# Performance work log

Measured on AMD Instinct MI355X. Metric: run time of the kernel, lower is better.

The kernel has to match this reference:

```python
import jax, jax.numpy as jnp
import numpy as np

N = 16384      # total nodes
B = 8          # graphs in batch
NPG = N // B   # nodes per graph
E = 262144     # edges
IN, HID, OUT = 128, 256, 128
ICP_ITERS = 10


def setup_inputs():
    key = jax.random.key(0)
    ks = jax.random.split(key, 12)
    x = jax.random.normal(ks[0], (N, IN), jnp.float32)
    # random edges kept within each graph (offsets per graph)
    src = jax.random.randint(ks[1], (E,), 0, NPG, dtype=jnp.int32)
    dst = jax.random.randint(ks[2], (E,), 0, NPG, dtype=jnp.int32)
    goff = (jnp.arange(E, dtype=jnp.int32) % B) * NPG
    edge_index = jnp.stack([src + goff, dst + goff], 0)
    pos = jax.random.normal(ks[3], (N, 3), jnp.float32)
    batch = jnp.repeat(jnp.arange(B, dtype=jnp.int32), NPG)
    def lin(k, fi, fo):
        return jax.random.normal(k, (fi, fo), jnp.float32) * (fi ** -0.5)
    return dict(
        x=x, edge_index=edge_index, pos=pos, batch=batch,
        W1=lin(ks[4], IN, HID),  b1=jnp.zeros((HID,), jnp.float32),
        W2=lin(ks[5], HID, HID), b2=jnp.zeros((HID,), jnp.float32),
        W3=lin(ks[6], HID, OUT), b3=jnp.zeros((OUT,), jnp.float32),
        Wt=lin(ks[7], OUT, 3),   bt=jnp.zeros((3,), jnp.float32),
    )


def gcn_conv(x, W, b, row, col, n):
    # GCNConv: symmetric norm with self loops; messages flow row->col
    xw = x @ W
    loop = jnp.arange(n, dtype=row.dtype)
    r = jnp.concatenate([row, loop])
    c = jnp.concatenate([col, loop])
    deg = jax.ops.segment_sum(jnp.ones_like(c, dtype=xw.dtype), c, num_segments=n)
    dinv = jnp.where(deg > 0, jax.lax.rsqrt(jnp.maximum(deg, 1e-12)), 0.0)
    norm = dinv[r] * dinv[c]
    out = jax.ops.segment_sum(xw[r] * norm[:, None], c, num_segments=n)
    return out + b


def pdist2(a, b):
    # squared pairwise distances [n,m]
    return (jnp.sum(a * a, -1)[:, None] + jnp.sum(b * b, -1)[None, :]
            - 2.0 * (a @ b.T))


def icp_align(src, tgt):
    # fixed-iteration batched ICP (Kabsch/SVD per iteration)
    for _ in range(ICP_ITERS):
        d = pdist2(jax.lax.stop_gradient(src), jax.lax.stop_gradient(tgt))
        idx = jnp.argmin(d, axis=1)
        corr = tgt[idx]
        cs = jnp.mean(src, 0)
        cc = jnp.mean(corr, 0)
        H = (src - cs).T @ (corr - cc)  # [3,3]
        U, S, Vt = jnp.linalg.svd(H, full_matrices=False)
        sign = jnp.sign(jnp.linalg.det(Vt.T @ U.T))
        D = jnp.stack([jnp.ones_like(sign), jnp.ones_like(sign), sign])
        R = (Vt.T * D[None, :]) @ U.T
        t = cc - R @ cs
        src = src @ R.T + t
    return src


def chamfer(a, b):
    d = pdist2(jax.lax.stop_gradient(a), jax.lax.stop_gradient(b))
    ia = jnp.argmin(d, 1)
    ib = jnp.argmin(d, 0)
    d1 = jnp.mean(jnp.sum((a - b[ia]) ** 2, -1))
    d2 = jnp.mean(jnp.sum((b - a[ib]) ** 2, -1))
    return d1 + d2


def reference(x, edge_index, pos, batch, W1, b1, W2, b2, W3, b3, Wt, bt):
    n = x.shape[0]
    row, col = edge_index[0], edge_index[1]
    h = jax.nn.relu(gcn_conv(x, W1, b1, row, col, n))
    h = jax.nn.relu(gcn_conv(h, W2, b2, row, col, n))
    h = gcn_conv(h, W3, b3, row, col, n)
    pos_offset = h @ Wt + bt
    tpos = pos + pos_offset
    nb = int(batch[-1]) + 1          # sorted, equal-size graphs
    npg = n // nb
    src = tpos.reshape(nb, npg, 3)
    tgt = pos.reshape(nb, npg, 3)
    aligned = jax.vmap(icp_align)(src, tgt)
    loss = jnp.mean(jax.vmap(chamfer)(aligned, tgt))
    return h, aligned.reshape(n, 3), loss
```

## Files before the change

### kernel.cpp

```cpp
#include <hip/hip_runtime.h>
#include <math.h>

#define N_NODES 16384
#define B_GRAPHS 8
#define NPG_     2048
#define E_EDGES  262144
#define F_IN  128
#define F_HID 256
#define F_OUT 128
#define ICP_IT 10
#define NN_BPG 32

typedef __attribute__((ext_vector_type(8))) short bf16x8;
typedef __attribute__((ext_vector_type(4))) float f32x4;

__device__ __forceinline__ float b2f(unsigned short u) {
    union { unsigned int u; float f; } v; v.u = ((unsigned int)u) << 16; return v.f;
}
__device__ __forceinline__ unsigned short f2b(float f) {
    union { float f; unsigned int u; } v; v.f = f;
    unsigned int r = v.u + 0x7FFFu + ((v.u >> 16) & 1u);
    return (unsigned short)(r >> 16);
}
__device__ __forceinline__ int swz32(int i) {
    return (i & ~31) | ((i & 31) ^ ((i >> 5) & 31));
}
__device__ __forceinline__ void st_agent(float* p, float v) {
    __hip_atomic_store(p, v, __ATOMIC_RELAXED, __HIP_MEMORY_SCOPE_AGENT);
}
__device__ __forceinline__ float ld_agent(const float* p) {
    return __hip_atomic_load(p, __ATOMIC_RELAXED, __HIP_MEMORY_SCOPE_AGENT);
}
__device__ __forceinline__ int ld_agent_i(const int* p) {
    return __hip_atomic_load(p, __ATOMIC_RELAXED, __HIP_MEMORY_SCOPE_AGENT);
}

__global__ __launch_bounds__(256) void k_prep(
    const float* __restrict__ x, unsigned short* __restrict__ xb,
    const float* __restrict__ W1, const float* __restrict__ W2, const float* __restrict__ W3,
    unsigned short* __restrict__ W1b, unsigned short* __restrict__ W2b, unsigned short* __restrict__ W3b,
    int* __restrict__ counts, int* __restrict__ ctrs)
{
    const int b = blockIdx.x, tid = threadIdx.x;
    if (b < 2048) {
        int i = b * 256 + tid;
        float4 v = ((const float4*)x)[i];
        uint2 o;
        o.x = (unsigned int)f2b(v.x) | ((unsigned int)f2b(v.y) << 16);
        o.y = (unsigned int)f2b(v.z) | ((unsigned int)f2b(v.w) << 16);
        ((uint2*)xb)[i] = o;
    } else if (b < 2176) {
        int idx = (b - 2048) * 256 + tid;
        int k = idx >> 8, n = idx & 255;
        W1b[n * 128 + k] = f2b(W1[idx]);
    } else if (b < 2432) {
        int idx = (b - 2176) * 256 + tid;
        int k = idx >> 8, n = idx & 255;
        W2b[n * 256 + k] = f2b(W2[idx]);
    } else if (b < 2560) {
        int idx = (b - 2432) * 256 + tid;
        int k = idx >> 7, n = idx & 127;
        W3b[n * 256 + k] = f2b(W3[idx]);
    } else if (b < 2576) {
        int i = (b - 2560) * 256 + tid;
        ((int4*)counts)[i] = make_int4(0, 0, 0, 0);
    } else {
        ctrs[tid] = 0;
    }
}

__global__ void k_count(const int* __restrict__ col, int* __restrict__ counts) {
    int e = blockIdx.x * 256 + threadIdx.x;
    if (e < E_EDGES) atomicAdd(&counts[col[e]], 1);
}

__global__ __launch_bounds__(1024) void k_scan(const int* __restrict__ counts,
        int* __restrict__ offs, int* __restrict__ cursor, float* __restrict__ dinv)
{
    __shared__ int wtot[16];
    const int t = threadIdx.x;
    const int base = t * 16;
    int local[16];
    int s = 0;
#pragma unroll
    for (int i = 0; i < 16; i++) { local[i] = counts[base + i]; s += local[i]; }
    const int lane = t & 63, w = t >> 6;
    int inc = s;
    for (int o = 1; o < 64; o <<= 1) {
        int v = __shfl_up(inc, o);
        if (lane >= o) inc += v;
    }
    if (lane == 63) wtot[w] = inc;
    __syncthreads();
    if (t < 16) {
        int v = wtot[t];
        for (int o = 1; o < 16; o <<= 1) {
            int u = __shfl_up(v, o);
            if (t >= o) v += u;
        }
        wtot[t] = v;
    }
    __syncthreads();
    int run = (w > 0 ? wtot[w - 1] : 0) + (inc - s);
#pragma unroll
    for (int i = 0; i < 16; i++) {
        offs[base + i]   = run;
        cursor[base + i] = run;
        dinv[base + i]   = rsqrtf((float)(local[i] + 1));
        run += local[i];
    }
    if (t == 1023) offs[N_NODES] = run;
}

__global__ void k_scatter(const int* __restrict__ row, const int* __restrict__ col,
        int* __restrict__ cursor, const float* __restrict__ dinv,
        int* __restrict__ srcid, float* __restrict__ normv)
{
    int e = blockIdx.x * 256 + threadIdx.x;
    if (e >= E_EDGES) return;
    int r = row[e], c = col[e];
    int p = atomicAdd(&cursor[c], 1);
    srcid[p] = r;
    normv[p] = dinv[r] * dinv[c];
}

template<int W, int OUTF, int FUSET>
__global__ __launch_bounds__(128) void k_agg(const unsigned short* __restrict__ X,
        void* __restrict__ Y,
        const int* __restrict__ offs, const int* __restrict__ srcid,
        const float* __restrict__ normv, const float* __restrict__ dinv,
        const float* __restrict__ bias, int relu,
        const float* __restrict__ Wt, const float* __restrict__ bt,
        const float* __restrict__ pos, float* __restrict__ tposO)
{
    constexpr int NPB = (W == 128) ? 2 : 1;
    constexpr int W2 = W / 2;
    const int local = (NPB == 2) ? (threadIdx.x >> 6) : 0;
    const int n = blockIdx.x * NPB + local;
    const int j = (NPB == 2) ? (threadIdx.x & 63) : threadIdx.x;
    const unsigned int* Xu = (const unsigned int*)X;
    float di = dinv[n];
    float w0 = di * di;
    unsigned int v = Xu[(size_t)n * W2 + j];
    float a0 = b2f((unsigned short)v) * w0;
    float a1 = b2f((unsigned short)(v >> 16)) * w0;
    int p = offs[n];
    const int p1 = offs[n + 1];
    for (; p + 3 < p1; p += 4) {
        int s0i = srcid[p], s1i = srcid[p + 1], s2i = srcid[p + 2], s3i = srcid[p + 3];
        float n0 = normv[p], n1 = normv[p + 1], n2 = normv[p + 2], n3 = normv[p + 3];
        unsigned int v0 = Xu[(size_t)s0i * W2 + j];
        unsigned int v1 = Xu[(size_t)s1i * W2 + j];
        unsigned int v2 = Xu[(size_t)s2i * W2 + j];
        unsigned int v3 = Xu[(size_t)s3i * W2 + j];
        a0 = fmaf(b2f((unsigned short)v0), n0, a0);
        a1 = fmaf(b2f((unsigned short)(v0 >> 16)), n0, a1);
        a0 = fmaf(b2f((unsigned short)v1), n1, a0);
        a1 = fmaf(b2f((unsigned short)(v1 >> 16)), n1, a1);
        a0 = fmaf(b2f((unsigned short)v2), n2, a0);
        a1 = fmaf(b2f((unsigned short)(v2 >> 16)), n2, a1);
        a0 = fmaf(b2f((unsigned short)v3), n3, a0);
        a1 = fmaf(b2f((unsigned short)(v3 >> 16)), n3, a1);
    }
    for (; p < p1; ++p) {
        unsigned int va = Xu[(size_t)srcid[p] * W2 + j]; float na = normv[p];
        a0 = fmaf(b2f((unsigned short)va), na, a0);
        a1 = fmaf(b2f((unsigned short)(va >> 16)), na, a1);
    }
    if (bias) { a0 += bias[2 * j]; a1 += bias[2 * j + 1]; }
    if (relu) { a0 = fmaxf(a0, 0.f); a1 = fmaxf(a1, 0.f); }
    if (OUTF) {
        float* Yf = (float*)Y;
        Yf[(size_t)n * W + 2 * j]     = a0;
        Yf[(size_t)n * W + 2 * j + 1] = a1;
    } else {
        ((unsigned int*)Y)[(size_t)n * W2 + j] =
            (unsigned int)f2b(a0) | ((unsigned int)f2b(a1) << 16);
    }
    if (FUSET) {
        float wt0 = Wt[6 * j + 0], wt1 = Wt[6 * j + 1], wt2 = Wt[6 * j + 2];
        float wt3 = Wt[6 * j + 3], wt4 = Wt[6 * j + 4], wt5 = Wt[6 * j + 5];
        float s0 = a0 * wt0 + a1 * wt3;
        float s1 = a0 * wt1 + a1 * wt4;
        float s2 = a0 * wt2 + a1 * wt5;
        for (int o = 32; o > 0; o >>= 1) {
            s0 += __shfl_down(s0, o);
            s1 += __shfl_down(s1, o);
            s2 += __shfl_down(s2, o);
        }
        if (j == 0) {
            tposO[n * 3 + 0] = pos[n * 3 + 0] + s0 + bt[0];
            tposO[n * 3 + 1] = pos[n * 3 + 1] + s1 + bt[1];
            tposO[n * 3 + 2] = pos[n * 3 + 2] + s2 + bt[2];
        }
    }
}

__global__ __launch_bounds__(256) void k_gemm_bf16(
    const unsigned short* __restrict__ A,
    const unsigned short* __restrict__ Bt,
    const float* __restrict__ bias, unsigned short* __restrict__ C,
    int M, int N, int K, int relu)
{
    __shared__ __align__(16) unsigned short As[128 * 64];
    __shared__ __align__(16) unsigned short Bs[64 * 64];
    const int tid  = threadIdx.x;
    const int lane = tid & 63;
    const int wave = tid >> 6;
    const int bm = blockIdx.y * 128, bn = blockIdx.x * 64;
    const int wm = (wave >> 1) * 64, wn = (wave & 1) * 32;
    f32x4 acc[4][2];
#pragma unroll
    for (int mf = 0; mf < 4; mf++)
#pragma unroll
        for (int nf = 0; nf < 2; nf++) acc[mf][nf] = (f32x4){0.f, 0.f, 0.f, 0.f};

    for (int k0 = 0; k0 < K; k0 += 64) {
#pragma unroll
        for (int i = 0; i < 4; i++) {
            int idx = i * 256 + tid;
            int m = idx >> 3, slot = idx & 7;
            const unsigned short* src = A + (size_t)(bm + m) * K + k0 + ((slot ^ (m & 7)) << 3);
            __builtin_amdgcn_global_load_lds(
                (const __attribute__((address_space(1))) unsigned int*)src,
                (__attribute__((address_space(3))) unsigned int*)(As + (size_t)i * 2048 + wave * 512),
                16, 0, 0);
        }
#pragma unroll
        for (int i = 0; i < 2; i++) {
            int idx = i * 256 + tid;
            int n = idx >> 3, slot = idx & 7;
            const unsigned short* src = Bt + (size_t)(bn + n) * K + k0 + ((slot ^ (n & 7)) << 3);
            __builtin_amdgcn_global_load_lds(
                (const __attribute__((address_space(1))) unsigned int*)src,
                (__attribute__((address_space(3))) unsigned int*)(Bs + (size_t)i * 2048 + wave * 512),
                16, 0, 0);
        }
        __syncthreads();
        bf16x8 af[4][2], bfr[2][2];
        const int qd = lane >> 4;
#pragma unroll
        for (int s = 0; s < 2; s++) {
#pragma unroll
            for (int mf = 0; mf < 4; mf++) {
                int m = wm + mf * 16 + (lane & 15);
                int slot = (s * 4 + qd) ^ (m & 7);
                af[mf][s] = *(const bf16x8*)(As + m * 64 + slot * 8);
            }
#pragma unroll
            for (int nf = 0; nf < 2; nf++) {
                int n = wn + nf * 16 + (lane & 15);
                int slot = (s * 4 + qd) ^ (n & 7);
                bfr[nf][s] = *(const bf16x8*)(Bs + n * 64 + slot * 8);
            }
        }
#pragma unroll
        for (int s = 0; s < 2; s++)
#pragma unroll
            for (int mf = 0; mf < 4; mf++)
#pragma unroll
                for (int nf = 0; nf < 2; nf++)
                    acc[mf][nf] = __builtin_amdgcn_mfma_f32_16x16x32_bf16(
                        af[mf][s], bfr[nf][s], acc[mf][nf], 0, 0, 0);
        __syncthreads();
    }
#pragma unroll
    for (int nf = 0; nf < 2; nf++) {
        int col = bn + wn + nf * 16 + (lane & 15);
        float bv = bias ? bias[col] : 0.f;
#pragma unroll
        for (int mf = 0; mf < 4; mf++) {
#pragma unroll
            for (int r = 0; r < 4; r++) {
                int row = bm + wm + mf * 16 + (lane >> 4) * 4 + r;
                float v = acc[mf][nf][r] + bv;
                if (relu) v = fmaxf(v, 0.f);
                C[(size_t)row * N + col] = f2b(v);
            }
        }
    }
}

__global__ __launch_bounds__(512) void k_icp_all(
    const float* __restrict__ tpos, const float* __restrict__ pos,
    float* __restrict__ partials,
    float* __restrict__ chpart,
    int* __restrict__ ctrs,
    float* __restrict__ out_aligned, float* __restrict__ out_loss)
{
    const int g = blockIdx.x >> 5, blk = blockIdx.x & 31;
    const int tid = threadIdx.x;
    const int wave = tid >> 6, lane = tid & 63;
    __shared__ float4 tq[NPG_];
    __shared__ __align__(16) unsigned char scratch[NPG_ * 16];
    float* sm_d = (float*)scratch;
    unsigned short* sm_i = (unsigned short*)(scratch + 64 * 65 * 4);
    float4* al = (float4*)scratch;
    __shared__ float mom[15][33];
    __shared__ float ssx[64], ssy[64], ssz[64];
    __shared__ float wred[16][2];
    __shared__ float Tsh[12];
    __shared__ double sdl[15];
    __shared__ int lastFlag;

    for (int i = tid; i < NPG_; i += 512) {
        const float* p = &pos[(size_t)(g * NPG_ + i) * 3];
        float qx = p[0], qy = p[1], qz = p[2];
        tq[swz32(i)] = make_float4(qx, qy, qz, fmaf(qx, qx, fmaf(qy, qy, qz * qz)));
    }
    if (tid < 12) Tsh[tid] = (tid == 0 || tid == 4 || tid == 8) ? 1.f : 0.f;
    float Px[8], Py[8], Pz[8];
#pragma unroll
    for (int u = 0; u < 8; u++) {
        int n = g * NPG_ + blk * 64 + wave * 8 + u;
        Px[u] = tpos[n * 3 + 0]; Py[u] = tpos[n * 3 + 1]; Pz[u] = tpos[n * 3 + 2];
    }
    double Td[12];
    if (tid == 0) {
#pragma unroll
        for (int k = 0; k < 12; k++) Td[k] = (k == 0 || k == 4 || k == 8) ? 1.0 : 0.0;
    }
    __syncthreads();

    for (int iter = 0; iter < ICP_IT; ++iter) {
        const int bufbase = (iter & 1) * 256;
        float Tf[12];
#pragma unroll
        for (int k = 0; k < 12; k++) Tf[k] = Tsh[k];
        float Sx[8], Sy[8], Sz[8], Tx[8], Ty[8], Tz[8], bd[8];
        int bi[8];
#pragma unroll
        for (int u = 0; u < 8; u++) {
            float X = Tf[0] * Px[u] + Tf[1] * Py[u] + Tf[2] * Pz[u] + Tf[9];
            float Y = Tf[3] * Px[u] + Tf[4] * Py[u] + Tf[5] * Pz[u] + Tf[10];
            float Z = Tf[6] * Px[u] + Tf[7] * Py[u] + Tf[8] * Pz[u] + Tf[11];
            Sx[u] = X; Sy[u] = Y; Sz[u] = Z;
            Tx[u] = -2.f * X; Ty[u] = -2.f * Y; Tz[u] = -2.f * Z;
            bd[u] = 1e30f; bi[u] = lane * 32;
        }
        const int qbase = lane * 32;
        for (int j = 0; j < 32; j++) {
            float4 t4 = tq[qbase + (j ^ (lane & 31))];
            int idx = qbase + j;
#pragma unroll
            for (int u = 0; u < 8; u++) {
                float d = fmaf(Tx[u], t4.x, fmaf(Ty[u], t4.y, fmaf(Tz[u], t4.z, t4.w)));
                if (d < bd[u]) { bd[u] = d; bi[u] = idx; }
            }
        }
#pragma unroll
        for (int u = 0; u < 8; u++) {
            int rowoff = (wave * 8 + u) * 65;
            sm_d[rowoff + lane] = bd[u];
            sm_i[rowoff + lane] = (unsigned short)bi[u];
            if (lane == u) { ssx[wave * 8 + u] = Sx[u]; ssy[wave * 8 + u] = Sy[u]; ssz[wave * 8 + u] = Sz[u]; }
        }
        __syncthreads();
        if (tid < 64) {
            const int s = tid;
            float best = sm_d[s * 65];
            int ib = sm_i[s * 65];
            for (int r = 1; r < 64; r++) {
                float dd = sm_d[s * 65 + r];
                int ii = sm_i[s * 65 + r];
                if (dd < best) { best = dd; ib = ii; }
            }
            float4 c = tq[swz32(ib)];
            float X = ssx[s], Y = ssy[s], Z = ssz[s];
            float vals[15] = { X, Y, Z, c.x, c.y, c.z,
                               X * c.x, X * c.y, X * c.z,
                               Y * c.x, Y * c.y, Y * c.z,
                               Z * c.x, Z * c.y, Z * c.z };
#pragma unroll
            for (int k = 0; k < 15; k++) {
                float v = vals[k];
                for (int o = 32; o > 0; o >>= 1) v += __shfl_down(v, o);
                if (tid == 0) st_agent(&partials[((size_t)bufbase + blockIdx.x) * 16 + k], v);
            }
        }
        __syncthreads();
        if (tid == 0) {
            atomicAdd(&ctrs[g * 16], 1);
            const int target = 32 * (iter + 1);
            while (ld_agent_i(&ctrs[g * 16]) < target) __builtin_amdgcn_s_sleep(8);
        }
        __syncthreads();
        if (tid < 480) {
            int kk = tid >> 5, bb = tid & 31;
            mom[kk][bb] = ld_agent(&partials[((size_t)bufbase + g * 32 + bb) * 16 + kk]);
        }
        __syncthreads();
        if (tid < 15) {
            double acc = 0;
            for (int b = 0; b < NN_BPG; b++) acc += (double)mom[tid][b];
            sdl[tid] = acc;
        }
        __syncthreads();
        if (tid == 0) {
            double sd[15];
#pragma unroll
            for (int k = 0; k < 15; k++) sd[k] = sdl[k];
            const double n = (double)NPG_;
            const double rin = 1.0 / (double)NPG_;
            double cs0 = sd[0] * rin, cs1 = sd[1] * rin, cs2 = sd[2] * rin;
            double cc0 = sd[3] * rin, cc1 = sd[4] * rin, cc2 = sd[5] * rin;
            float H[3][3];
            H[0][0] = (float)(sd[6]  - n * cs0 * cc0); H[0][1] = (float)(sd[7]  - n * cs0 * cc1); H[0][2] = (float)(sd[8]  - n * cs0 * cc2);
            H[1][0] = (float)(sd[9]  - n * cs1 * cc0); H[1][1] = (float)(sd[10] - n * cs1 * cc1); H[1][2] = (float)(sd[11] - n * cs1 * cc2);
            H[2][0] = (float)(sd[12] - n * cs2 * cc0); H[2][1] = (float)(sd[13] - n * cs2 * cc1); H[2][2] = (float)(sd[14] - n * cs2 * cc2);
            double R[3][3];
            float fn = 1e-30f;
            for (int i = 0; i < 3; i++) for (int j2 = 0; j2 < 3; j2++) fn += H[i][j2] * H[i][j2];
            float sc = rsqrtf(fn);
            float Xm[3][3];
            for (int i = 0; i < 3; i++) for (int j2 = 0; j2 < 3; j2++) Xm[i][j2] = H[i][j2] * sc;
            float dX = Xm[0][0] * (Xm[1][1]*Xm[2][2] - Xm[1][2]*Xm[2][1])
                     - Xm[0][1] * (Xm[1][0]*Xm[2][2] - Xm[1][2]*Xm[2][0])
                     + Xm[0][2] * (Xm[1][0]*Xm[2][1] - Xm[1][1]*Xm[2][0]);
            if (dX > 1e-4f) {
                for (int itn = 0; itn < 24; ++itn) {
                    float C00 = Xm[1][1]*Xm[2][2] - Xm[1][2]*Xm[2][1];
                    float C01 = Xm[1][2]*Xm[2][0] - Xm[1][0]*Xm[2][2];
                    float C02 = Xm[1][0]*Xm[2][1] - Xm[1][1]*Xm[2][0];
                    float C10 = Xm[2][1]*Xm[0][2] - Xm[2][2]*Xm[0][1];
                    float C11 = Xm[2][2]*Xm[0][0] - Xm[2][0]*Xm[0][2];
                    float C12 = Xm[2][0]*Xm[0][1] - Xm[2][1]*Xm[0][0];
                    float C20 = Xm[0][1]*Xm[1][2] - Xm[0][2]*Xm[1][1];
                    float C21 = Xm[0][2]*Xm[1][0] - Xm[0][0]*Xm[1][2];
                    float C22 = Xm[0][0]*Xm[1][1] - Xm[0][1]*Xm[1][0];
                    float det = Xm[0][0]*C00 + Xm[0][1]*C01 + Xm[0][2]*C02;
                    if (fabsf(det) < 1e-30f) break;
                    float rd = 0.5f / det;
                    Xm[0][0] = 0.5f*Xm[0][0] + C00*rd; Xm[0][1] = 0.5f*Xm[0][1] + C01*rd; Xm[0][2] = 0.5f*Xm[0][2] + C02*rd;
                    Xm[1][0] = 0.5f*Xm[1][0] + C10*rd; Xm[1][1] = 0.5f*Xm[1][1] + C11*rd; Xm[1][2] = 0.5f*Xm[1][2] + C12*rd;
                    Xm[2][0] = 0.5f*Xm[2][0] + C20*rd; Xm[2][1] = 0.5f*Xm[2][1] + C21*rd; Xm[2][2] = 0.5f*Xm[2][2] + C22*rd;
                }
                for (int i = 0; i < 3; i++) for (int j2 = 0; j2 < 3; j2++) R[i][j2] = (double)Xm[j2][i];
            } else {
                float A[3][3], V[3][3] = {{1,0,0},{0,1,0},{0,0,1}};
                for (int i = 0; i < 3; i++)
                    for (int j2 = 0; j2 < 3; j2++)
                        A[i][j2] = H[0][i] * H[0][j2] + H[1][i] * H[1][j2] + H[2][i] * H[2][j2];
                for (int sweep = 0; sweep < 8; ++sweep) {
                    for (int p = 0; p < 2; p++) for (int q = p + 1; q < 3; q++) {
                        float apq = A[p][q];
                        if (fabsf(apq) < 1e-30f) continue;
                        float theta = (A[q][q] - A[p][p]) / (2.f * apq);
                        float t = copysignf(1.f, theta) / (fabsf(theta) + sqrtf(theta * theta + 1.f));
                        float c = 1.f / sqrtf(t * t + 1.f);
                        float s = t * c;
                        for (int k = 0; k < 3; k++) { float akp = A[k][p], akq = A[k][q]; A[k][p] = c*akp - s*akq; A[k][q] = s*akp + c*akq; }
                        for (int k = 0; k < 3; k++) { float apk = A[p][k], aqk = A[q][k]; A[p][k] = c*apk - s*aqk; A[q][k] = s*apk + c*aqk; }
                        for (int k = 0; k < 3; k++) { float vkp = V[k][p], vkq = V[k][q]; V[k][p] = c*vkp - s*vkq; V[k][q] = s*vkp + c*vkq; }
                    }
                }
                float lam[3] = { A[0][0], A[1][1], A[2][2] };
                int ord[3] = { 0, 1, 2 };
                if (lam[ord[1]] > lam[ord[0]]) { int t0 = ord[0]; ord[0] = ord[1]; ord[1] = t0; }
                if (lam[ord[2]] > lam[ord[0]]) { int t0 = ord[0]; ord[0] = ord[2]; ord[2] = t0; }
                if (lam[ord[2]] > lam[ord[1]]) { int t0 = ord[1]; ord[1] = ord[2]; ord[2] = t0; }
                float vc[3][3], uc[3][3];
                for (int i = 0; i < 3; i++) { vc[i][0] = V[0][ord[i]]; vc[i][1] = V[1][ord[i]]; vc[i][2] = V[2][ord[i]]; }
                for (int i = 0; i < 3; i++) {
                    float u0 = H[0][0]*vc[i][0] + H[0][1]*vc[i][1] + H[0][2]*vc[i][2];
                    float u1 = H[1][0]*vc[i][0] + H[1][1]*vc[i][1] + H[1][2]*vc[i][2];
                    float u2 = H[2][0]*vc[i][0] + H[2][1]*vc[i][1] + H[2][2]*vc[i][2];
                    for (int j2 = 0; j2 < i; j2++) {
                        float dp = u0*uc[j2][0] + u1*uc[j2][1] + u2*uc[j2][2];
                        u0 -= dp*uc[j2][0]; u1 -= dp*uc[j2][1]; u2 -= dp*uc[j2][2];
                    }
                    float nn2 = sqrtf(u0*u0 + u1*u1 + u2*u2);
                    if (nn2 > 1e-12f) { uc[i][0] = u0/nn2; uc[i][1] = u1/nn2; uc[i][2] = u2/nn2; }
                    else if (i == 2) {
                        uc[2][0] = uc[0][1]*uc[1][2] - uc[0][2]*uc[1][1];
                        uc[2][1] = uc[0][2]*uc[1][0] - uc[0][0]*uc[1][2];
                        uc[2][2] = uc[0][0]*uc[1][1] - uc[0][1]*uc[1][0];
                    } else if (i == 1) {
                        float a0 = (fabsf(uc[0][0]) < 0.9f) ? 1.f : 0.f, a1 = 1.f - a0, a2 = 0.f;
                        float dp = a0*uc[0][0] + a1*uc[0][1] + a2*uc[0][2];
                        a0 -= dp*uc[0][0]; a1 -= dp*uc[0][1]; a2 -= dp*uc[0][2];
                        float nn3 = sqrtf(a0*a0 + a1*a1 + a2*a2);
                        uc[1][0] = a0/nn3; uc[1][1] = a1/nn3; uc[1][2] = a2/nn3;
                    } else { uc[0][0] = 1; uc[0][1] = 0; uc[0][2] = 0; }
                }
                float detU = uc[0][0]*(uc[1][1]*uc[2][2] - uc[1][2]*uc[2][1])
                           - uc[0][1]*(uc[1][0]*uc[2][2] - uc[1][2]*uc[2][0])
                           + uc[0][2]*(uc[1][0]*uc[2][1] - uc[1][1]*uc[2][0]);
                float detV = vc[0][0]*(vc[1][1]*vc[2][2] - vc[1][2]*vc[2][1])
                           - vc[0][1]*(vc[1][0]*vc[2][2] - vc[1][2]*vc[2][0])
                           + vc[0][2]*(vc[1][0]*vc[2][1] - vc[1][1]*vc[2][0]);
                float sgn = (detU * detV < 0.f) ? -1.f : 1.f;
                for (int i = 0; i < 3; i++)
                    for (int j2 = 0; j2 < 3; j2++)
                        R[i][j2] = (double)(vc[0][i]*uc[0][j2] + vc[1][i]*uc[1][j2] + sgn * vc[2][i]*uc[2][j2]);
            }
            double tr0 = cc0 - (R[0][0]*cs0 + R[0][1]*cs1 + R[0][2]*cs2);
            double tr1 = cc1 - (R[1][0]*cs0 + R[1][1]*cs1 + R[1][2]*cs2);
            double tr2 = cc2 - (R[2][0]*cs0 + R[2][1]*cs1 + R[2][2]*cs2);
            double An[12];
            for (int i = 0; i < 3; i++)
                for (int j2 = 0; j2 < 3; j2++)
                    An[i*3+j2] = R[i][0]*Td[0*3+j2] + R[i][1]*Td[1*3+j2] + R[i][2]*Td[2*3+j2];
            An[9]  = R[0][0]*Td[9] + R[0][1]*Td[10] + R[0][2]*Td[11] + tr0;
            An[10] = R[1][0]*Td[9] + R[1][1]*Td[10] + R[1][2]*Td[11] + tr1;
            An[11] = R[2][0]*Td[9] + R[2][1]*Td[10] + R[2][2]*Td[11] + tr2;
#pragma unroll
            for (int k = 0; k < 12; k++) { Td[k] = An[k]; Tsh[k] = (float)An[k]; }
        }
        __syncthreads();
    }

    {
        float Tf[12];
#pragma unroll
        for (int k = 0; k < 12; k++) Tf[k] = Tsh[k];
        __syncthreads();
        for (int i = tid; i < NPG_; i += 512) {
            const float* q = &tpos[(size_t)(g * NPG_ + i) * 3];
            float X = Tf[0] * q[0] + Tf[1] * q[1] + Tf[2] * q[2] + Tf[9];
            float Y = Tf[3] * q[0] + Tf[4] * q[1] + Tf[5] * q[2] + Tf[10];
            float Z = Tf[6] * q[0] + Tf[7] * q[1] + Tf[8] * q[2] + Tf[11];
            al[swz32(i)] = make_float4(X, Y, Z, fmaf(X, X, fmaf(Y, Y, Z * Z)));
            if (blk == 0) {
                out_aligned[(size_t)(g * NPG_ + i) * 3 + 0] = X;
                out_aligned[(size_t)(g * NPG_ + i) * 3 + 1] = Y;
                out_aligned[(size_t)(g * NPG_ + i) * 3 + 2] = Z;
            }
        }
        __syncthreads();
        float Ax[8], Ay[8], Az[8], Aw[8], Qx[8], Qy[8], Qz[8], Qw[8], d1[8], d2[8];
#pragma unroll
        for (int u = 0; u < 8; u++) {
            int s = swz32(blk * 64 + wave * 8 + u);
            float4 a4 = al[s]; float4 p4 = tq[s];
            Ax[u] = -2.f * a4.x; Ay[u] = -2.f * a4.y; Az[u] = -2.f * a4.z; Aw[u] = a4.w;
            Qx[u] = -2.f * p4.x; Qy[u] = -2.f * p4.y; Qz[u] = -2.f * p4.z; Qw[u] = p4.w;
            d1[u] = 1e30f; d2[u] = 1e30f;
        }
        const int qbase = lane * 32;
        for (int j = 0; j < 32; j++) {
            int s = qbase + (j ^ (lane & 31));
            float4 t4 = tq[s];
            float4 b4 = al[s];
#pragma unroll
            for (int u = 0; u < 8; u++) {
                d1[u] = fminf(d1[u], fmaf(Ax[u], t4.x, fmaf(Ay[u], t4.y, fmaf(Az[u], t4.z, t4.w))));
                d2[u] = fminf(d2[u], fmaf(Qx[u], b4.x, fmaf(Qy[u], b4.y, fmaf(Qz[u], b4.z, b4.w))));
            }
        }
        float s1 = 0.f, s2 = 0.f;
#pragma unroll
        for (int u = 0; u < 8; u++) {
            float a = d1[u], b = d2[u];
            for (int o = 32; o > 0; o >>= 1) {
                a = fminf(a, __shfl_down(a, o));
                b = fminf(b, __shfl_down(b, o));
            }
            s1 += a + Aw[u];
            s2 += b + Qw[u];
        }
        if (lane == 0) { wred[wave][0] = s1; wred[wave][1] = s2; }
        __syncthreads();
        if (tid == 0) {
            float t1 = 0.f, t2 = 0.f;
#pragma unroll
            for (int w = 0; w < 8; w++) { t1 += wred[w][0]; t2 += wred[w][1]; }
            st_agent(&chpart[blockIdx.x * 2 + 0], t1);
            st_agent(&chpart[blockIdx.x * 2 + 1], t2);
        }
        __syncthreads();
        if (tid == 0) {
            int old = atomicAdd(&ctrs[128], 1);
            lastFlag = (old == (int)gridDim.x - 1) ? 1 : 0;
        }
        __syncthreads();
        if (!lastFlag) return;
        float v1 = 0.f, v2 = 0.f;
        if (tid < 256) {
            v1 = ld_agent(&chpart[tid * 2 + 0]);
            v2 = ld_agent(&chpart[tid * 2 + 1]);
        }
        for (int o = 32; o > 0; o >>= 1) {
            v1 += __shfl_down(v1, o);
            v2 += __shfl_down(v2, o);
        }
        if (lane == 0 && wave < 4) { wred[wave][0] = v1; wred[wave][1] = v2; }
        __syncthreads();
        if (tid == 0) {
            float tot = 0.f;
#pragma unroll
            for (int w = 0; w < 4; w++) tot += wred[w][0] + wred[w][1];
            out_loss[0] = tot / (float)(NPG_ * B_GRAPHS);
        }
    }
}

extern "C" void kernel_launch(void* const* d_in, const int* in_sizes, int n_in,
                              void* d_out, int out_size, void* d_ws, size_t ws_size,
                              hipStream_t stream)
{
    (void)in_sizes; (void)n_in; (void)out_size; (void)ws_size;
    const float* x   = (const float*)d_in[0];
    const int*   ei  = (const int*)d_in[1];
    const float* pos = (const float*)d_in[2];
    const float* W1 = (const float*)d_in[4];
    const float* b1 = (const float*)d_in[5];
    const float* W2 = (const float*)d_in[6];
    const float* b2 = (const float*)d_in[7];
    const float* W3 = (const float*)d_in[8];
    const float* b3 = (const float*)d_in[9];
    const float* Wt = (const float*)d_in[10];
    const float* bt = (const float*)d_in[11];
    const int* row = ei;
    const int* col = ei + E_EDGES;

    char* wsb = (char*)d_ws;
    size_t off_b = 0;
    auto alloc = [&](size_t bytes) -> void* {
        void* p = wsb + off_b;
        off_b = (off_b + bytes + 255) & ~(size_t)255;
        return p;
    };
    int*    counts   = (int*)alloc((size_t)N_NODES * 4);
    int*    offs     = (int*)alloc((size_t)(N_NODES + 1) * 4);
    int*    cursor   = (int*)alloc((size_t)N_NODES * 4);
    int*    srcid    = (int*)alloc((size_t)E_EDGES * 4);
    float*  normv    = (float*)alloc((size_t)E_EDGES * 4);
    float*  dinv     = (float*)alloc((size_t)N_NODES * 4);
    unsigned short* xb  = (unsigned short*)alloc((size_t)N_NODES * F_IN * 2);
    unsigned short* W1b = (unsigned short*)alloc((size_t)F_IN * F_HID * 2);
    unsigned short* W2b = (unsigned short*)alloc((size_t)F_HID * F_HID * 2);
    unsigned short* W3b = (unsigned short*)alloc((size_t)F_HID * F_OUT * 2);
    unsigned short* bufA = (unsigned short*)alloc((size_t)N_NODES * F_HID * 2);
    unsigned short* bufB = (unsigned short*)alloc((size_t)N_NODES * F_HID * 2);
    unsigned short* bufC = (unsigned short*)alloc((size_t)N_NODES * F_HID * 2);
    float*  tpos     = (float*)alloc((size_t)N_NODES * 3 * 4);
    float*  partials = (float*)alloc((size_t)2 * 256 * 16 * 4);
    int*    ctrs     = (int*)alloc((size_t)256 * 4);
    float*  chpart   = (float*)alloc((size_t)256 * 2 * 4);

    float* out_h       = (float*)d_out;
    float* out_aligned = out_h + (size_t)N_NODES * F_OUT;
    float* out_loss    = out_aligned + (size_t)N_NODES * 3;

    k_prep<<<2577, 256, 0, stream>>>(x, xb, W1, W2, W3, W1b, W2b, W3b, counts, ctrs);
    k_count<<<E_EDGES / 256, 256, 0, stream>>>(col, counts);
    k_scan<<<1, 1024, 0, stream>>>(counts, offs, cursor, dinv);
    k_scatter<<<E_EDGES / 256, 256, 0, stream>>>(row, col, cursor, dinv, srcid, normv);

    k_agg<F_IN, 0, 0><<<N_NODES / 2, 128, 0, stream>>>(xb, bufA, offs, srcid, normv, dinv,
            nullptr, 0, nullptr, nullptr, nullptr, nullptr);
    {
        dim3 grid(F_HID / 64, N_NODES / 128);
        k_gemm_bf16<<<grid, 256, 0, stream>>>(bufA, W1b, b1, bufB, N_NODES, F_HID, F_IN, 1);
    }
    {
        dim3 grid(F_HID / 64, N_NODES / 128);
        k_gemm_bf16<<<grid, 256, 0, stream>>>(bufB, W2b, nullptr, bufC, N_NODES, F_HID, F_HID, 0);
    }
    k_agg<F_HID, 0, 0><<<N_NODES, 128, 0, stream>>>(bufC, bufA, offs, srcid, normv, dinv,
            b2, 1, nullptr, nullptr, nullptr, nullptr);
    {
        dim3 grid(F_OUT / 64, N_NODES / 128);
        k_gemm_bf16<<<grid, 256, 0, stream>>>(bufA, W3b, nullptr, bufB, N_NODES, F_OUT, F_HID, 0);
    }
    k_agg<F_OUT, 1, 1><<<N_NODES / 2, 128, 0, stream>>>(bufB, out_h, offs, srcid, normv, dinv,
            b3, 0, Wt, bt, pos, tpos);

    k_icp_all<<<B_GRAPHS * NN_BPG, 512, 0, stream>>>(tpos, pos, partials, chpart, ctrs,
            out_aligned, out_loss);
}
```

Baseline: 330.8 us.

## Fuse degree counting into prep kernel and streamline ICP cross-block reduction

Edge degree counting moves into the prep kernel, and the counts buffer is zeroed with an async memset. This removes one kernel launch. In the ICP kernel, partial moments are now written with plain stores plus threadfences instead of atomic stores, read back with float4 vector loads in the natural layout, and the spin-wait sleep is shortened. The polar-decomposition Newton iterations drop from 24 to 16, which may lower rotation accuracy when convergence is slow.

Result: slower. 373.2 us (+12.8%).

```diff
diff --git a/kernel.cpp b/kernel.cpp
--- a/kernel.cpp
+++ b/kernel.cpp
@@ -39,7 +39,7 @@
     const float* __restrict__ x, unsigned short* __restrict__ xb,
     const float* __restrict__ W1, const float* __restrict__ W2, const float* __restrict__ W3,
     unsigned short* __restrict__ W1b, unsigned short* __restrict__ W2b, unsigned short* __restrict__ W3b,
-    int* __restrict__ counts, int* __restrict__ ctrs)
+    const int* __restrict__ col, int* __restrict__ counts, int* __restrict__ ctrs)
 {
     const int b = blockIdx.x, tid = threadIdx.x;
     if (b < 2048) {
@@ -61,17 +61,12 @@
         int idx = (b - 2432) * 256 + tid;
         int k = idx >> 7, n = idx & 127;
         W3b[n * 256 + k] = f2b(W3[idx]);
-    } else if (b < 2576) {
-        int i = (b - 2560) * 256 + tid;
-        ((int4*)counts)[i] = make_int4(0, 0, 0, 0);
+    } else if (b < 3584) {
+        int e = (b - 2560) * 256 + tid;
+        atomicAdd(&counts[col[e]], 1);
     } else {
         ctrs[tid] = 0;
     }
-}
-
-__global__ void k_count(const int* __restrict__ col, int* __restrict__ counts) {
-    int e = blockIdx.x * 256 + threadIdx.x;
-    if (e < E_EDGES) atomicAdd(&counts[col[e]], 1);
 }
 
 __global__ __launch_bounds__(1024) void k_scan(const int* __restrict__ counts,
@@ -296,9 +291,9 @@
     float* sm_d = (float*)scratch;
     unsigned short* sm_i = (unsigned short*)(scratch + 64 * 65 * 4);
     float4* al = (float4*)scratch;
-    __shared__ float mom[15][33];
+    __shared__ __align__(16) float pmom[32][16];
     __shared__ float ssx[64], ssy[64], ssz[64];
-    __shared__ float wred[16][2];
+    __shared__ float wred[8][2];
     __shared__ float Tsh[12];
     __shared__ double sdl[15];
     __shared__ int lastFlag;
@@ -350,10 +345,10 @@
         }
 #pragma unroll
         for (int u = 0; u < 8; u++) {
-            int rowoff = (wave * 8 + u) * 65;
-            sm_d[rowoff + lane] = bd[u];
-            sm_i[rowoff + lane] = (unsigned short)bi[u];
-            if (lane == u) { ssx[wave * 8 + u] = Sx[u]; ssy[wave * 8 + u] = Sy[u]; ssz[wave * 8 + u] = Sz[u]; }
+            int row = wave * 8 + u;
+            sm_d[row * 65 + lane] = bd[u];
+            sm_i[row * 65 + lane] = (unsigned short)bi[u];
+            if (lane == u) { ssx[row] = Sx[u]; ssy[row] = Sy[u]; ssz[row] = Sz[u]; }
         }
         __syncthreads();
         if (tid < 64) {
@@ -375,24 +370,26 @@
             for (int k = 0; k < 15; k++) {
                 float v = vals[k];
                 for (int o = 32; o > 0; o >>= 1) v += __shfl_down(v, o);
-                if (tid == 0) st_agent(&partials[((size_t)bufbase + blockIdx.x) * 16 + k], v);
+                if (tid == 0) partials[((size_t)bufbase + blockIdx.x) * 16 + k] = v;
             }
         }
         __syncthreads();
         if (tid == 0) {
+            __threadfence();
             atomicAdd(&ctrs[g * 16], 1);
             const int target = 32 * (iter + 1);
-            while (ld_agent_i(&ctrs[g * 16]) < target) __builtin_amdgcn_s_sleep(8);
-        }
-        __syncthreads();
-        if (tid < 480) {
-            int kk = tid >> 5, bb = tid & 31;
-            mom[kk][bb] = ld_agent(&partials[((size_t)bufbase + g * 32 + bb) * 16 + kk]);
+            while (ld_agent_i(&ctrs[g * 16]) < target) __builtin_amdgcn_s_sleep(2);
+            __threadfence();
+        }
+        __syncthreads();
+        if (tid < 128) {
+            const float4* src = (const float4*)(partials + ((size_t)bufbase + g * 32) * 16);
+            ((float4*)pmom)[tid] = src[tid];
         }
         __syncthreads();
         if (tid < 15) {
             double acc = 0;
-            for (int b = 0; b < NN_BPG; b++) acc += (double)mom[tid][b];
+            for (int b = 0; b < NN_BPG; b++) acc += (double)pmom[b][tid];
             sdl[tid] = acc;
         }
         __syncthreads();
@@ -418,7 +415,7 @@
                      - Xm[0][1] * (Xm[1][0]*Xm[2][2] - Xm[1][2]*Xm[2][0])
                      + Xm[0][2] * (Xm[1][0]*Xm[2][1] - Xm[1][1]*Xm[2][0]);
             if (dX > 1e-4f) {
-                for (int itn = 0; itn < 24; ++itn) {
+                for (int itn = 0; itn < 16; ++itn) {
                     float C00 = Xm[1][1]*Xm[2][2] - Xm[1][2]*Xm[2][1];
                     float C01 = Xm[1][2]*Xm[2][0] - Xm[1][0]*Xm[2][2];
                     float C02 = Xm[1][0]*Xm[2][1] - Xm[1][1]*Xm[2][0];
@@ -643,8 +640,8 @@
     float* out_aligned = out_h + (size_t)N_NODES * F_OUT;
     float* out_loss    = out_aligned + (size_t)N_NODES * 3;
 
-    k_prep<<<2577, 256, 0, stream>>>(x, xb, W1, W2, W3, W1b, W2b, W3b, counts, ctrs);
-    k_count<<<E_EDGES / 256, 256, 0, stream>>>(col, counts);
+    hipMemsetAsync(counts, 0, (size_t)N_NODES * 4, stream);
+    k_prep<<<3585, 256, 0, stream>>>(x, xb, W1, W2, W3, W1b, W2b, W3b, col, counts, ctrs);
     k_scan<<<1, 1024, 0, stream>>>(counts, offs, cursor, dinv);
     k_scatter<<<E_EDGES / 256, 256, 0, stream>>>(row, col, cursor, dinv, srcid, normv);
 
```
